# Kernel tuning notes

Hardware: AMD Instinct MI355X
Metric: run time of the kernel (lower is better)

Reference implementation:

```python
import jax, jax.numpy as jnp
import numpy as np

N_LAYERS = 4
H = 16
LOOKBACK = 128  # cross_window
EPS = 1e-6
ROPE_BASE = 10000.0
NEG = jnp.float32(-1e30)


def rmsnorm(x, w):
    return x * jax.lax.rsqrt(jnp.mean(x * x, axis=-1, keepdims=True) + EPS) * w


def rope_cache(L, hd):
    inv = 1.0 / (ROPE_BASE ** (jnp.arange(0, hd, 2, dtype=jnp.float32) / hd))
    t = jnp.arange(L, dtype=jnp.float32)
    f = t[:, None] * inv[None, :]            # [L, hd/2]
    emb = jnp.concatenate([f, f], axis=-1)   # [L, hd]
    return jnp.cos(emb), jnp.sin(emb)


def apply_rope(x, cos, sin):
    # x: [B,H,L,d]; rotate-half convention
    d = x.shape[-1]
    x1, x2 = x[..., : d // 2], x[..., d // 2:]
    rot = jnp.concatenate([-x2, x1], axis=-1)
    return x * cos + rot * sin


def split_heads(x, n_heads):
    B, L, D = x.shape
    return x.reshape(B, L, n_heads, D // n_heads).transpose(0, 2, 1, 3)


def merge_heads(x):
    B, h, L, d = x.shape
    return x.transpose(0, 2, 1, 3).reshape(B, L, h * d)


def sdpa(q, k, v, bias):
    scale = q.shape[-1] ** -0.5
    s = jnp.einsum('bhqd,bhkd->bhqk', q, k) * scale + bias
    p = jax.nn.softmax(s, axis=-1)
    return jnp.einsum('bhqk,bhkd->bhqd', p, v)


def forward(x, memory, seg_ids, Wqkv, bqkv, Wo, bo, Wq_c, Wkv_c, Wo_c, Wg, Wu, Wd, n1, n2, n3, nf):
    B, L, D = x.shape
    S = memory.shape[1]
    hd = D // H
    cos, sin = rope_cache(L, hd)

    # causal additive mask [1,1,L,L]
    i = jnp.arange(L)
    causal_bias = jnp.where(i[None, :] <= i[:, None], 0.0, NEG)[None, None]

    # segment-causal sliding-window cross mask [B,1,L,S]:
    # token t may attend memory j with seg_id[t]-LOOKBACK < j <= seg_id[t]
    j = jnp.arange(S)
    allowed = (j[None, None, :] <= seg_ids[:, :, None]) & (j[None, None, :] > seg_ids[:, :, None] - LOOKBACK)
    cross_bias = jnp.where(allowed, 0.0, NEG)[:, None]  # [B,1,L,S]

    for l in range(N_LAYERS):
        # --- causal self-attn with RoPE ---
        h = rmsnorm(x, n1[l])
        qkv = h @ Wqkv[l].T + bqkv[l]                      # [B,L,3D]
        q, k, v = jnp.split(qkv, 3, axis=-1)
        q = apply_rope(split_heads(q, H), cos, sin)
        k = apply_rope(split_heads(k, H), cos, sin)
        v = split_heads(v, H)
        o = merge_heads(sdpa(q, k, v, causal_bias)) @ Wo[l].T + bo[l]
        x = x + o

        # --- segment-causal sliding-window cross-attn ---
        h2 = rmsnorm(x, n2[l])
        qc = split_heads(h2 @ Wq_c[l].T, H)
        kv = memory @ Wkv_c[l].T                           # [B,S,2D]
        kc, vc = jnp.split(kv, 2, axis=-1)
        kc, vc = split_heads(kc, H), split_heads(vc, H)
        oc = merge_heads(sdpa(qc, kc, vc, cross_bias)) @ Wo_c[l].T
        x = x + oc

        # --- SwiGLU FFN ---
        h3 = rmsnorm(x, n3[l])
        x = x + (jax.nn.silu(h3 @ Wg[l].T) * (h3 @ Wu[l].T)) @ Wd[l].T

    return rmsnorm(x, nf)


def setup_inputs() -> dict:
    key = jax.random.key(0)
    ks = jax.random.split(key, 16)
    B, L, S, D, F = 2, 2048, 256, 1024, 4096
    w = 0.02
    inp = {
        'x': jax.random.normal(ks[0], (B, L, D), jnp.float32),
        'memory': jax.random.normal(ks[1], (B, S, D), jnp.float32),
        'seg_ids': jnp.sort(jax.random.randint(ks[2], (B, L), 0, S), axis=-1),
        'Wqkv': jax.random.normal(ks[3], (N_LAYERS, 3 * D, D), jnp.float32) * w,
        'bqkv': jnp.zeros((N_LAYERS, 3 * D), jnp.float32),
        'Wo': jax.random.normal(ks[4], (N_LAYERS, D, D), jnp.float32) * w,
        'bo': jnp.zeros((N_LAYERS, D), jnp.float32),
        'Wq_c': jax.random.normal(ks[5], (N_LAYERS, D, D), jnp.float32) * w,
        'Wkv_c': jax.random.normal(ks[6], (N_LAYERS, 2 * D, D), jnp.float32) * w,
        'Wo_c': jax.random.normal(ks[7], (N_LAYERS, D, D), jnp.float32) * w,
        'Wg': jax.random.normal(ks[8], (N_LAYERS, F, D), jnp.float32) * w,
        'Wu': jax.random.normal(ks[9], (N_LAYERS, F, D), jnp.float32) * w,
        'Wd': jax.random.normal(ks[10], (N_LAYERS, D, F), jnp.float32) * w,
        'n1': jnp.ones((N_LAYERS, D), jnp.float32),
        'n2': jnp.ones((N_LAYERS, D), jnp.float32),
        'n3': jnp.ones((N_LAYERS, D), jnp.float32),
        'nf': jnp.ones((D,), jnp.float32),
    }
    return inp


def reference(x, memory, seg_ids, Wqkv, bqkv, Wo, bo, Wq_c, Wkv_c, Wo_c, Wg, Wu, Wd, n1, n2, n3, nf):
    return forward(x, memory, seg_ids, Wqkv, bqkv, Wo, bo, Wq_c, Wkv_c, Wo_c, Wg, Wu, Wd, n1, n2, n3, nf)
```

## Files before the change

### kernel.cpp

```cpp
#include <hip/hip_runtime.h>
#include <hip/hip_bf16.h>
#include <math.h>

#define N_LAYERS 4
#define NHEADS 16
#define LOOKBACK 128

typedef unsigned short ushort_t;
typedef __attribute__((ext_vector_type(8))) short short8;
typedef __attribute__((ext_vector_type(4))) float f32x4;

__device__ __forceinline__ ushort_t f2bf(float f) {
    union { float f; unsigned int u; } v; v.f = f;
    unsigned int r = (v.u + 0x7FFFu + ((v.u >> 16) & 1u)) >> 16;
    return (ushort_t)r;
}
__device__ __forceinline__ float bf2f(ushort_t s) {
    union { unsigned int u; float f; } v; v.u = ((unsigned int)s) << 16;
    return v.f;
}

__device__ __forceinline__ float blk_sum(float v, volatile float* red) {
#pragma unroll
    for (int o = 32; o > 0; o >>= 1) v += __shfl_down(v, o, 64);
    if ((threadIdx.x & 63) == 0) red[threadIdx.x >> 6] = v;
    __syncthreads();
    float r = red[0] + red[1] + red[2] + red[3];
    __syncthreads();
    return r;
}

__global__ __launch_bounds__(256) void f2b_k(const float* __restrict__ in,
                                             ushort_t* __restrict__ out, int n4) {
    int i = blockIdx.x * 256 + threadIdx.x;
    if (i >= n4) return;
    float4 v = *(const float4*)(in + (size_t)i * 4);
    ushort_t* o = out + (size_t)i * 4;
    o[0] = f2bf(v.x); o[1] = f2bf(v.y); o[2] = f2bf(v.z); o[3] = f2bf(v.w);
}

__global__ __launch_bounds__(256) void rmsnorm_bf(const float* __restrict__ x,
                                                  const float* __restrict__ w,
                                                  ushort_t* __restrict__ out, int D) {
    __shared__ float red[4];
    size_t row = blockIdx.x;
    const float* xr = x + row * D;
    float ss = 0.f;
    for (int i = threadIdx.x; i < D; i += 256) { float v = xr[i]; ss += v * v; }
    float tot = blk_sum(ss, red);
    float r = rsqrtf(tot / (float)D + 1e-6f);
    ushort_t* o = out + row * D;
    for (int i = threadIdx.x; i < D; i += 256) o[i] = f2bf(xr[i] * r * w[i]);
}

__global__ __launch_bounds__(256) void rmsnorm_k(const float* __restrict__ x,
                                                 const float* __restrict__ w,
                                                 float* __restrict__ out, int D) {
    __shared__ float red[4];
    size_t row = blockIdx.x;
    const float* xr = x + row * D;
    float ss = 0.f;
    for (int i = threadIdx.x; i < D; i += 256) { float v = xr[i]; ss += v * v; }
    float tot = blk_sum(ss, red);
    float r = rsqrtf(tot / (float)D + 1e-6f);
    float* o = out + row * D;
    for (int i = threadIdx.x; i < D; i += 256) o[i] = xr[i] * r * w[i];
}

#define GBM 128
#define GBN 128
#define GBK 32

__global__ __launch_bounds__(256) void gemm_bf16(
    const ushort_t* __restrict__ A, const ushort_t* __restrict__ Bw,
    void* __restrict__ Cout, const float* __restrict__ bias,
    const float* __restrict__ resid, const ushort_t* __restrict__ gate,
    int M, int N, int K, int out_bf16) {
    __shared__ ushort_t As[GBM * GBK];
    __shared__ ushort_t Bs[GBN * GBK];
    int tid = threadIdx.x;
    int wave = tid >> 6, lane = tid & 63;
    int bm = blockIdx.y * GBM, bn = blockIdx.x * GBN;
    int wm = (wave & 1) * 64, wn = (wave >> 1) * 64;
    int r4 = lane >> 2, c4 = lane & 3;
    int r = lane & 15, q = lane >> 4;

    f32x4 acc[4][4];
#pragma unroll
    for (int i = 0; i < 4; ++i)
#pragma unroll
        for (int j = 0; j < 4; ++j) acc[i][j] = (f32x4){0.f, 0.f, 0.f, 0.f};

    int srow = wave * 16 + r4;
    for (int k0 = 0; k0 < K; k0 += GBK) {
        const ushort_t* Ag = A + (size_t)(bm + srow) * K + k0 + c4 * 8;
        const ushort_t* Bg = Bw + (size_t)(bn + srow) * K + k0 + c4 * 8;
        __builtin_amdgcn_global_load_lds(
            (const __attribute__((address_space(1))) void*)Ag,
            (__attribute__((address_space(3))) void*)&As[wave * 16 * GBK],
            16, 0, 0);
        __builtin_amdgcn_global_load_lds(
            (const __attribute__((address_space(1))) void*)(Ag + (size_t)64 * K),
            (__attribute__((address_space(3))) void*)&As[(64 + wave * 16) * GBK],
            16, 0, 0);
        __builtin_amdgcn_global_load_lds(
            (const __attribute__((address_space(1))) void*)Bg,
            (__attribute__((address_space(3))) void*)&Bs[wave * 16 * GBK],
            16, 0, 0);
        __builtin_amdgcn_global_load_lds(
            (const __attribute__((address_space(1))) void*)(Bg + (size_t)64 * K),
            (__attribute__((address_space(3))) void*)&Bs[(64 + wave * 16) * GBK],
            16, 0, 0);
        __syncthreads();
        short8 af[4], bfr[4];
#pragma unroll
        for (int i = 0; i < 4; ++i)
            af[i] = *(const short8*)&As[(wm + 16 * i + r) * GBK + q * 8];
#pragma unroll
        for (int j = 0; j < 4; ++j)
            bfr[j] = *(const short8*)&Bs[(wn + 16 * j + r) * GBK + q * 8];
#pragma unroll
        for (int i = 0; i < 4; ++i)
#pragma unroll
            for (int j = 0; j < 4; ++j)
                acc[i][j] = __builtin_amdgcn_mfma_f32_16x16x32_bf16(
                    af[i], bfr[j], acc[i][j], 0, 0, 0);
        __syncthreads();
    }
#pragma unroll
    for (int i = 0; i < 4; ++i) {
#pragma unroll
        for (int j = 0; j < 4; ++j) {
            size_t n = (size_t)(bn + wn + 16 * j + r);
            float bn_v = bias ? bias[n] : 0.f;
#pragma unroll
            for (int t = 0; t < 4; ++t) {
                size_t m = (size_t)(bm + wm + 16 * i + q * 4 + t);
                size_t idx = m * N + n;
                float x = acc[i][j][t] + bn_v;
                if (gate) { float g = bf2f(gate[idx]); x *= g / (1.0f + __expf(-g)); }
                if (resid) x += resid[idx];
                if (out_bf16) ((ushort_t*)Cout)[idx] = f2bf(x);
                else ((float*)Cout)[idx] = x;
            }
        }
    }
}

__global__ void rope_k(ushort_t* __restrict__ qkv, int L, int total) {
    int idx = blockIdx.x * 256 + threadIdx.x;
    if (idx >= total) return;
    int d = idx & 31;
    int h = (idx >> 5) & 15;
    int bl = idx >> 9;
    int l = bl % L;
    float inv = powf(10000.0f, -(float)d * (1.0f / 32.0f));
    float f = (float)l * inv;
    float s, c;
    sincosf(f, &s, &c);
    ushort_t* base = qkv + (size_t)bl * 3072 + h * 64 + d;
    float x1 = bf2f(base[0]), x2 = bf2f(base[32]);
    base[0]  = f2bf((x1 * c - x2 * s) * 0.125f);
    base[32] = f2bf((x2 * c + x1 * s) * 0.125f);
    ushort_t* kb = base + 1024;
    x1 = bf2f(kb[0]); x2 = bf2f(kb[32]);
    kb[0]  = f2bf(x1 * c - x2 * s);
    kb[32] = f2bf(x2 * c + x1 * s);
}

#define AP 72

__global__ __launch_bounds__(256) void self_attn_flash(
    const ushort_t* __restrict__ qkv, ushort_t* __restrict__ out, int L) {
    int qt = blockIdx.x, h = blockIdx.y, b = blockIdx.z;
    int q0 = qt * 64;
    __shared__ ushort_t Qs[64 * AP];
    __shared__ ushort_t Ks[64 * AP];
    __shared__ ushort_t VT[64 * AP];
    __shared__ ushort_t Ps[64 * AP];
    int tid = threadIdx.x;
    int wave = tid >> 6, lane = tid & 63;
    int g = lane >> 4, r = lane & 15;
    int lr = tid >> 2, lc = tid & 3;

    {
        const ushort_t* src = qkv + ((size_t)b * L + q0 + lr) * 3072 + h * 64 + lc * 16;
        *(short8*)&Qs[lr * AP + lc * 16]     = *(const short8*)(src);
        *(short8*)&Qs[lr * AP + lc * 16 + 8] = *(const short8*)(src + 8);
    }

    float m[4]    = {-1e30f, -1e30f, -1e30f, -1e30f};
    float lsum[4] = {0.f, 0.f, 0.f, 0.f};
    f32x4 acc[4];
#pragma unroll
    for (int j = 0; j < 4; ++j) acc[j] = (f32x4){0.f, 0.f, 0.f, 0.f};

    for (int kt = 0; kt <= qt; ++kt) {
        int k0 = kt * 64;
        __syncthreads();
        {
            const ushort_t* ksrc = qkv + ((size_t)b * L + k0 + lr) * 3072 + 1024 + h * 64 + lc * 16;
            short8 k0v = *(const short8*)(ksrc);
            short8 k1v = *(const short8*)(ksrc + 8);
            *(short8*)&Ks[lr * AP + lc * 16]     = k0v;
            *(short8*)&Ks[lr * AP + lc * 16 + 8] = k1v;
            const ushort_t* vsrc = ksrc + 1024;
            short8 v0v = *(const short8*)(vsrc);
            short8 v1v = *(const short8*)(vsrc + 8);
#pragma unroll
            for (int i = 0; i < 8; ++i) {
                VT[(lc * 16 + i) * AP + lr]     = (ushort_t)v0v[i];
                VT[(lc * 16 + 8 + i) * AP + lr] = (ushort_t)v1v[i];
            }
        }
        __syncthreads();

        f32x4 s[4];
#pragma unroll
        for (int j = 0; j < 4; ++j) s[j] = (f32x4){0.f, 0.f, 0.f, 0.f};
        short8 aq[2];
#pragma unroll
        for (int c = 0; c < 2; ++c)
            aq[c] = *(const short8*)&Qs[(wave * 16 + r) * AP + c * 32 + g * 8];
#pragma unroll
        for (int j = 0; j < 4; ++j)
#pragma unroll
            for (int c = 0; c < 2; ++c) {
                short8 bk = *(const short8*)&Ks[(16 * j + r) * AP + c * 32 + g * 8];
                s[j] = __builtin_amdgcn_mfma_f32_16x16x32_bf16(aq[c], bk, s[j], 0, 0, 0);
            }

        if (kt == qt) {
#pragma unroll
            for (int j = 0; j < 4; ++j)
#pragma unroll
                for (int t = 0; t < 4; ++t)
                    if (16 * j + r > 16 * wave + 4 * g + t) s[j][t] = -1e30f;
        }

        float al[4];
#pragma unroll
        for (int t = 0; t < 4; ++t) {
            float rm = fmaxf(fmaxf(s[0][t], s[1][t]), fmaxf(s[2][t], s[3][t]));
#pragma unroll
            for (int o = 8; o > 0; o >>= 1) rm = fmaxf(rm, __shfl_xor(rm, o, 16));
            float mn = fmaxf(m[t], rm);
            al[t] = __expf(m[t] - mn);
            m[t] = mn;
            float rs = 0.f;
#pragma unroll
            for (int j = 0; j < 4; ++j) {
                float p = __expf(s[j][t] - mn);
                s[j][t] = p;
                rs += p;
            }
#pragma unroll
            for (int o = 8; o > 0; o >>= 1) rs += __shfl_xor(rs, o, 16);
            lsum[t] = lsum[t] * al[t] + rs;
        }

        ushort_t* pw = &Ps[wave * 16 * AP];
#pragma unroll
        for (int j = 0; j < 4; ++j)
#pragma unroll
            for (int t = 0; t < 4; ++t)
                pw[(4 * g + t) * AP + 16 * j + r] = f2bf(s[j][t]);
        short8 ap[2];
#pragma unroll
        for (int c = 0; c < 2; ++c)
            ap[c] = *(const short8*)&pw[r * AP + c * 32 + g * 8];

#pragma unroll
        for (int j = 0; j < 4; ++j) {
#pragma unroll
            for (int t = 0; t < 4; ++t) acc[j][t] *= al[t];
#pragma unroll
            for (int c = 0; c < 2; ++c) {
                short8 bv = *(const short8*)&VT[(16 * j + r) * AP + c * 32 + g * 8];
                acc[j] = __builtin_amdgcn_mfma_f32_16x16x32_bf16(ap[c], bv, acc[j], 0, 0, 0);
            }
        }
    }

#pragma unroll
    for (int t = 0; t < 4; ++t) {
        float invl = 1.0f / lsum[t];
        size_t orow = ((size_t)b * L + q0 + wave * 16 + 4 * g + t) * 1024 + h * 64;
#pragma unroll
        for (int j = 0; j < 4; ++j)
            out[orow + 16 * j + r] = f2bf(acc[j][t] * invl);
    }
}

__global__ __launch_bounds__(256) void cross_attn_mfma(
    const ushort_t* __restrict__ qc, const ushort_t* __restrict__ kvc,
    const int* __restrict__ seg_ids, ushort_t* __restrict__ out, int L, int S) {
    int qt = blockIdx.x, h = blockIdx.y, b = blockIdx.z;
    int q0 = qt * 64;
    __shared__ ushort_t Qs[64 * AP];
    __shared__ ushort_t Ks[64 * AP];
    __shared__ ushort_t VT[64 * AP];
    __shared__ ushort_t Ps[64 * AP];
    __shared__ int segs[64];
    __shared__ int bounds[2];
    int tid = threadIdx.x;
    int wave = tid >> 6, lane = tid & 63;
    int g = lane >> 4, r = lane & 15;
    int lr = tid >> 2, lc = tid & 3;

    {
        const ushort_t* src = qc + ((size_t)b * L + q0 + lr) * 1024 + h * 64 + lc * 16;
        *(short8*)&Qs[lr * AP + lc * 16]     = *(const short8*)(src);
        *(short8*)&Qs[lr * AP + lc * 16 + 8] = *(const short8*)(src + 8);
    }
    if (tid < 64) segs[tid] = seg_ids[(size_t)b * L + q0 + tid];
    __syncthreads();
    if (wave == 0) {
        int v = segs[lane];
        int mn = v, mx = v;
#pragma unroll
        for (int o = 32; o > 0; o >>= 1) {
            mn = min(mn, __shfl_down(mn, o, 64));
            mx = max(mx, __shfl_down(mx, o, 64));
        }
        if (lane == 0) { bounds[0] = mn; bounds[1] = mx; }
    }
    int seg_t[4];
#pragma unroll
    for (int t = 0; t < 4; ++t) seg_t[t] = segs[wave * 16 + 4 * g + t];
    short8 aq[2];
#pragma unroll
    for (int c = 0; c < 2; ++c)
        aq[c] = *(const short8*)&Qs[(wave * 16 + r) * AP + c * 32 + g * 8];
    __syncthreads();
    int lo = bounds[0] - (LOOKBACK - 1); if (lo < 0) lo = 0;
    int t_lo = lo >> 6;
    int t_hi = bounds[1] >> 6;

    float m[4]    = {-1e30f, -1e30f, -1e30f, -1e30f};
    float lsum[4] = {0.f, 0.f, 0.f, 0.f};
    f32x4 acc[4];
#pragma unroll
    for (int j = 0; j < 4; ++j) acc[j] = (f32x4){0.f, 0.f, 0.f, 0.f};

    for (int kt = t_lo; kt <= t_hi; ++kt) {
        int k0 = kt * 64;
        __syncthreads();
        {
            const ushort_t* ksrc = kvc + ((size_t)b * S + k0 + lr) * 2048 + h * 64 + lc * 16;
            short8 k0v = *(const short8*)(ksrc);
            short8 k1v = *(const short8*)(ksrc + 8);
            *(short8*)&Ks[lr * AP + lc * 16]     = k0v;
            *(short8*)&Ks[lr * AP + lc * 16 + 8] = k1v;
            const ushort_t* vsrc = ksrc + 1024;
            short8 v0v = *(const short8*)(vsrc);
            short8 v1v = *(const short8*)(vsrc + 8);
#pragma unroll
            for (int i = 0; i < 8; ++i) {
                VT[(lc * 16 + i) * AP + lr]     = (ushort_t)v0v[i];
                VT[(lc * 16 + 8 + i) * AP + lr] = (ushort_t)v1v[i];
            }
        }
        __syncthreads();

        f32x4 s[4];
#pragma unroll
        for (int j = 0; j < 4; ++j) s[j] = (f32x4){0.f, 0.f, 0.f, 0.f};
#pragma unroll
        for (int j = 0; j < 4; ++j)
#pragma unroll
            for (int c = 0; c < 2; ++c) {
                short8 bk = *(const short8*)&Ks[(16 * j + r) * AP + c * 32 + g * 8];
                s[j] = __builtin_amdgcn_mfma_f32_16x16x32_bf16(aq[c], bk, s[j], 0, 0, 0);
            }

#pragma unroll
        for (int j = 0; j < 4; ++j) {
            int k = k0 + 16 * j + r;
#pragma unroll
            for (int t = 0; t < 4; ++t) {
                float v = s[j][t] * 0.125f;
                if (k > seg_t[t] || k <= seg_t[t] - LOOKBACK) v = -1e30f;
                s[j][t] = v;
            }
        }

        float al[4];
#pragma unroll
        for (int t = 0; t < 4; ++t) {
            float rm = fmaxf(fmaxf(s[0][t], s[1][t]), fmaxf(s[2][t], s[3][t]));
#pragma unroll
            for (int o = 8; o > 0; o >>= 1) rm = fmaxf(rm, __shfl_xor(rm, o, 16));
            float mn = fmaxf(m[t], rm);
            al[t] = __expf(m[t] - mn);
            m[t] = mn;
            float rs = 0.f;
#pragma unroll
            for (int j = 0; j < 4; ++j) {
                float p = __expf(s[j][t] - mn);
                s[j][t] = p;
                rs += p;
            }
#pragma unroll
            for (int o = 8; o > 0; o >>= 1) rs += __shfl_xor(rs, o, 16);
            lsum[t] = lsum[t] * al[t] + rs;
        }

        ushort_t* pw = &Ps[wave * 16 * AP];
#pragma unroll
        for (int j = 0; j < 4; ++j)
#pragma unroll
            for (int t = 0; t < 4; ++t)
                pw[(4 * g + t) * AP + 16 * j + r] = f2bf(s[j][t]);
        short8 ap[2];
#pragma unroll
        for (int c = 0; c < 2; ++c)
            ap[c] = *(const short8*)&pw[r * AP + c * 32 + g * 8];

#pragma unroll
        for (int j = 0; j < 4; ++j) {
#pragma unroll
            for (int t = 0; t < 4; ++t) acc[j][t] *= al[t];
#pragma unroll
            for (int c = 0; c < 2; ++c) {
                short8 bv = *(const short8*)&VT[(16 * j + r) * AP + c * 32 + g * 8];
                acc[j] = __builtin_amdgcn_mfma_f32_16x16x32_bf16(ap[c], bv, acc[j], 0, 0, 0);
            }
        }
    }

#pragma unroll
    for (int t = 0; t < 4; ++t) {
        float invl = 1.0f / lsum[t];
        size_t orow = ((size_t)b * L + q0 + wave * 16 + 4 * g + t) * 1024 + h * 64;
#pragma unroll
        for (int j = 0; j < 4; ++j)
            out[orow + 16 * j + r] = f2bf(acc[j][t] * invl);
    }
}

extern "C" void kernel_launch(void* const* d_in, const int* in_sizes, int n_in,
                              void* d_out, int out_size, void* d_ws, size_t ws_size,
                              hipStream_t stream) {
    const int B = 2, L = 2048, S = 256, D = 1024, F = 4096;
    const int BL = B * L;
    const float* x_in   = (const float*)d_in[0];
    const float* memory = (const float*)d_in[1];
    const int*   seg    = (const int*)d_in[2];
    const float* Wqkv = (const float*)d_in[3];
    const float* bqkv = (const float*)d_in[4];
    const float* Wo   = (const float*)d_in[5];
    const float* bo   = (const float*)d_in[6];
    const float* Wq_c = (const float*)d_in[7];
    const float* Wkv_c= (const float*)d_in[8];
    const float* Wo_c = (const float*)d_in[9];
    const float* Wg   = (const float*)d_in[10];
    const float* Wu   = (const float*)d_in[11];
    const float* Wd   = (const float*)d_in[12];
    const float* n1   = (const float*)d_in[13];
    const float* n2   = (const float*)d_in[14];
    const float* n3   = (const float*)d_in[15];
    const float* nf   = (const float*)d_in[16];

    char* ws = (char*)d_ws;
    size_t off = 0;
    float* X     = (float*)(ws + off); off += (size_t)BL * D * 4;
    float* QKV   = (float*)(ws + off); off += (size_t)BL * 3 * D * 4;
    float* KVC   = (float*)(ws + off); off += (size_t)B * S * 2 * D * 4;
    ushort_t* Hn  = (ushort_t*)(ws + off); off += (size_t)BL * D * 2;
    ushort_t* Abf = (ushort_t*)(ws + off); off += (size_t)BL * D * 2;
    ushort_t* Mb  = (ushort_t*)(ws + off); off += (size_t)B * S * D * 2;
    ushort_t* Wb  = (ushort_t*)(ws + off); off += (size_t)F * D * 2;
    ushort_t* QKVb = (ushort_t*)QKV;
    ushort_t* Qcb  = (ushort_t*)QKV;
    ushort_t* KVCb = (ushort_t*)KVC;
    ushort_t* Gg = (ushort_t*)QKV;

    hipMemcpyAsync(X, x_in, (size_t)BL * D * sizeof(float), hipMemcpyDeviceToDevice, stream);

    dim3 blk(256);
    f2b_k<<<(B * S * D / 4 + 255) / 256, blk, 0, stream>>>(memory, Mb, B * S * D / 4);

    for (int l = 0; l < N_LAYERS; ++l) {
        rmsnorm_bf<<<BL, blk, 0, stream>>>(X, n1 + (size_t)l * D, Hn, D);
        f2b_k<<<(3 * D * D / 4 + 255) / 256, blk, 0, stream>>>(
            Wqkv + (size_t)l * 3 * D * D, Wb, 3 * D * D / 4);
        gemm_bf16<<<dim3(3 * D / GBN, BL / GBM), blk, 0, stream>>>(
            Hn, Wb, QKVb, bqkv + (size_t)l * 3 * D, nullptr, nullptr, BL, 3 * D, D, 1);
        int total = BL * NHEADS * 32;
        rope_k<<<(total + 255) / 256, blk, 0, stream>>>(QKVb, L, total);
        self_attn_flash<<<dim3(L / 64, NHEADS, B), blk, 0, stream>>>(QKVb, Abf, L);
        f2b_k<<<(D * D / 4 + 255) / 256, blk, 0, stream>>>(
            Wo + (size_t)l * D * D, Wb, D * D / 4);
        gemm_bf16<<<dim3(D / GBN, BL / GBM), blk, 0, stream>>>(
            Abf, Wb, X, bo + (size_t)l * D, X, nullptr, BL, D, D, 0);
        rmsnorm_bf<<<BL, blk, 0, stream>>>(X, n2 + (size_t)l * D, Hn, D);
        f2b_k<<<(D * D / 4 + 255) / 256, blk, 0, stream>>>(
            Wq_c + (size_t)l * D * D, Wb, D * D / 4);
        gemm_bf16<<<dim3(D / GBN, BL / GBM), blk, 0, stream>>>(
            Hn, Wb, Qcb, nullptr, nullptr, nullptr, BL, D, D, 1);
        f2b_k<<<(2 * D * D / 4 + 255) / 256, blk, 0, stream>>>(
            Wkv_c + (size_t)l * 2 * D * D, Wb, 2 * D * D / 4);
        gemm_bf16<<<dim3(2 * D / GBN, B * S / GBM), blk, 0, stream>>>(
            Mb, Wb, KVCb, nullptr, nullptr, nullptr, B * S, 2 * D, D, 1);
        cross_attn_mfma<<<dim3(L / 64, NHEADS, B), blk, 0, stream>>>(
            Qcb, KVCb, seg, Abf, L, S);
        f2b_k<<<(D * D / 4 + 255) / 256, blk, 0, stream>>>(
            Wo_c + (size_t)l * D * D, Wb, D * D / 4);
        gemm_bf16<<<dim3(D / GBN, BL / GBM), blk, 0, stream>>>(
            Abf, Wb, X, nullptr, X, nullptr, BL, D, D, 0);
        rmsnorm_bf<<<BL, blk, 0, stream>>>(X, n3 + (size_t)l * D, Hn, D);
        f2b_k<<<(F * D / 4 + 255) / 256, blk, 0, stream>>>(
            Wg + (size_t)l * F * D, Wb, F * D / 4);
        gemm_bf16<<<dim3(F / GBN, BL / GBM), blk, 0, stream>>>(
            Hn, Wb, Gg, nullptr, nullptr, nullptr, BL, F, D, 1);
        f2b_k<<<(F * D / 4 + 255) / 256, blk, 0, stream>>>(
            Wu + (size_t)l * F * D, Wb, F * D / 4);
        gemm_bf16<<<dim3(F / GBN, BL / GBM), blk, 0, stream>>>(
            Hn, Wb, Gg, nullptr, nullptr, Gg, BL, F, D, 1);
        f2b_k<<<(D * F / 4 + 255) / 256, blk, 0, stream>>>(
            Wd + (size_t)l * D * F, Wb, D * F / 4);
        gemm_bf16<<<dim3(D / GBN, BL / GBM), blk, 0, stream>>>(
            Gg, Wb, X, nullptr, X, nullptr, BL, D, F, 0);
    }
    rmsnorm_k<<<BL, blk, 0, stream>>>(X, nf, (float*)d_out, D);
}
```

Measured before the change: 3.021 ms.

## Enlarge self-attention query tile, prefetch KV, swizzle LDS, and remap blocks to XCDs

The self-attention kernel now processes 128 query rows per block, with each wave owning 32 rows, so every K/V tile loaded into LDS is reused twice as much. The next K/V tile is prefetched into registers while the current one is consumed, and the V-transpose and P buffers use XOR-swizzled layouts instead of padding to reduce LDS bank conflicts. Block indices in both the GEMM and the attention kernel are remapped so that neighbouring tiles land on the same XCD for L2 locality. RoPE's powf is replaced with exp2f. The attention remap hardcodes 16 query tiles and 16 heads, which ties it to L=2048, and the larger tile halves the number of attention blocks while raising register pressure.

```diff
diff --git a/kernel.cpp b/kernel.cpp
--- a/kernel.cpp
+++ b/kernel.cpp
@@ -80,7 +80,12 @@
     __shared__ ushort_t Bs[GBN * GBK];
     int tid = threadIdx.x;
     int wave = tid >> 6, lane = tid & 63;
-    int bm = blockIdx.y * GBM, bn = blockIdx.x * GBN;
+    int nwg = gridDim.x * gridDim.y;
+    int wg  = blockIdx.y * gridDim.x + blockIdx.x;
+    int qq = nwg >> 3, rr = nwg & 7;
+    int xcd = wg & 7, loc = wg >> 3;
+    int swz = (xcd < rr ? xcd * (qq + 1) : rr * (qq + 1) + (xcd - rr) * qq) + loc;
+    int bm = (swz / gridDim.x) * GBM, bn = (swz % gridDim.x) * GBN;
     int wm = (wave & 1) * 64, wn = (wave >> 1) * 64;
     int r4 = lane >> 2, c4 = lane & 3;
     int r = lane & 15, q = lane >> 4;
@@ -154,7 +159,7 @@
     int h = (idx >> 5) & 15;
     int bl = idx >> 9;
     int l = bl % L;
-    float inv = powf(10000.0f, -(float)d * (1.0f / 32.0f));
+    float inv = exp2f(-(float)d * (13.2877123795f / 32.0f));
     float f = (float)l * inv;
     float s, c;
     sincosf(f, &s, &c);
@@ -168,129 +173,185 @@
     kb[32] = f2bf(x2 * c + x1 * s);
 }
 
-#define AP 72
+#define QB 128
 
 __global__ __launch_bounds__(256) void self_attn_flash(
     const ushort_t* __restrict__ qkv, ushort_t* __restrict__ out, int L) {
-    int qt = blockIdx.x, h = blockIdx.y, b = blockIdx.z;
-    int q0 = qt * 64;
-    __shared__ ushort_t Qs[64 * AP];
-    __shared__ ushort_t Ks[64 * AP];
-    __shared__ ushort_t VT[64 * AP];
-    __shared__ ushort_t Ps[64 * AP];
+    int lin = blockIdx.x + gridDim.x * (blockIdx.y + gridDim.y * blockIdx.z);
+    int xcd = lin & 7, slot = lin >> 3;
+    int qt = slot & 15;
+    int grp = xcd + 8 * (slot >> 4);
+    int h = grp & 15, b = grp >> 4;
+    int q0 = qt * QB;
+
+    __shared__ ushort_t Qs[QB * 72];
+    __shared__ ushort_t Ks[64 * 72];
+    __shared__ ushort_t VT[64 * 64];
+    __shared__ ushort_t Ps[QB * 64];
+
     int tid = threadIdx.x;
     int wave = tid >> 6, lane = tid & 63;
     int g = lane >> 4, r = lane & 15;
+    int lr2 = tid >> 1, lc2 = tid & 1;
     int lr = tid >> 2, lc = tid & 3;
 
     {
-        const ushort_t* src = qkv + ((size_t)b * L + q0 + lr) * 3072 + h * 64 + lc * 16;
-        *(short8*)&Qs[lr * AP + lc * 16]     = *(const short8*)(src);
-        *(short8*)&Qs[lr * AP + lc * 16 + 8] = *(const short8*)(src + 8);
-    }
-
-    float m[4]    = {-1e30f, -1e30f, -1e30f, -1e30f};
-    float lsum[4] = {0.f, 0.f, 0.f, 0.f};
-    f32x4 acc[4];
-#pragma unroll
-    for (int j = 0; j < 4; ++j) acc[j] = (f32x4){0.f, 0.f, 0.f, 0.f};
-
-    for (int kt = 0; kt <= qt; ++kt) {
+        const ushort_t* src = qkv + ((size_t)b * L + q0 + lr2) * 3072 + h * 64 + lc2 * 32;
+        ushort_t* dst = &Qs[lr2 * 72 + lc2 * 32];
+        *(short8*)(dst)      = *(const short8*)(src);
+        *(short8*)(dst + 8)  = *(const short8*)(src + 8);
+        *(short8*)(dst + 16) = *(const short8*)(src + 16);
+        *(short8*)(dst + 24) = *(const short8*)(src + 24);
+    }
+    __syncthreads();
+    short8 aq[2][2];
+#pragma unroll
+    for (int s = 0; s < 2; ++s)
+#pragma unroll
+        for (int c = 0; c < 2; ++c)
+            aq[s][c] = *(const short8*)&Qs[(wave * 32 + s * 16 + r) * 72 + c * 32 + g * 8];
+
+    const ushort_t* kvbase = qkv + ((size_t)b * L + lr) * 3072 + 1024 + h * 64 + lc * 16;
+    short8 kreg0 = *(const short8*)(kvbase);
+    short8 kreg1 = *(const short8*)(kvbase + 8);
+    short8 vreg0 = *(const short8*)(kvbase + 1024);
+    short8 vreg1 = *(const short8*)(kvbase + 1032);
+
+    float m[2][4], lsum[2][4];
+    f32x4 acc[2][4];
+#pragma unroll
+    for (int s = 0; s < 2; ++s)
+#pragma unroll
+        for (int t = 0; t < 4; ++t) { m[s][t] = -1e30f; lsum[s][t] = 0.f; }
+#pragma unroll
+    for (int s = 0; s < 2; ++s)
+#pragma unroll
+        for (int j = 0; j < 4; ++j) acc[s][j] = (f32x4){0.f, 0.f, 0.f, 0.f};
+
+    int ktmax = 2 * qt + 1;
+    for (int kt = 0; kt <= ktmax; ++kt) {
+        __syncthreads();
+        *(short8*)&Ks[lr * 72 + lc * 16]     = kreg0;
+        *(short8*)&Ks[lr * 72 + lc * 16 + 8] = kreg1;
+#pragma unroll
+        for (int i = 0; i < 8; ++i) {
+            int row0 = lc * 16 + i;
+            int f0 = (row0 & 7) ^ ((row0 >> 4) & 3);
+            VT[row0 * 64 + (((lr >> 3) ^ f0) << 3) + (lr & 7)] = (ushort_t)vreg0[i];
+            int row1 = row0 + 8;
+            int f1 = (row1 & 7) ^ ((row1 >> 4) & 3);
+            VT[row1 * 64 + (((lr >> 3) ^ f1) << 3) + (lr & 7)] = (ushort_t)vreg1[i];
+        }
+        if (kt < ktmax) {
+            const ushort_t* p = kvbase + (size_t)(kt + 1) * 64 * 3072;
+            kreg0 = *(const short8*)(p);
+            kreg1 = *(const short8*)(p + 8);
+            vreg0 = *(const short8*)(p + 1024);
+            vreg1 = *(const short8*)(p + 1032);
+        }
+        __syncthreads();
+
         int k0 = kt * 64;
-        __syncthreads();
-        {
-            const ushort_t* ksrc = qkv + ((size_t)b * L + k0 + lr) * 3072 + 1024 + h * 64 + lc * 16;
-            short8 k0v = *(const short8*)(ksrc);
-            short8 k1v = *(const short8*)(ksrc + 8);
-            *(short8*)&Ks[lr * AP + lc * 16]     = k0v;
-            *(short8*)&Ks[lr * AP + lc * 16 + 8] = k1v;
-            const ushort_t* vsrc = ksrc + 1024;
-            short8 v0v = *(const short8*)(vsrc);
-            short8 v1v = *(const short8*)(vsrc + 8);
-#pragma unroll
-            for (int i = 0; i < 8; ++i) {
-                VT[(lc * 16 + i) * AP + lr]     = (ushort_t)v0v[i];
-                VT[(lc * 16 + 8 + i) * AP + lr] = (ushort_t)v1v[i];
-            }
-        }
-        __syncthreads();
-
-        f32x4 s[4];
-#pragma unroll
-        for (int j = 0; j < 4; ++j) s[j] = (f32x4){0.f, 0.f, 0.f, 0.f};
-        short8 aq[2];
-#pragma unroll
-        for (int c = 0; c < 2; ++c)
-            aq[c] = *(const short8*)&Qs[(wave * 16 + r) * AP + c * 32 + g * 8];
+        f32x4 s2[2][4];
+#pragma unroll
+        for (int s = 0; s < 2; ++s)
+#pragma unroll
+            for (int j = 0; j < 4; ++j) s2[s][j] = (f32x4){0.f, 0.f, 0.f, 0.f};
 #pragma unroll
         for (int j = 0; j < 4; ++j)
 #pragma unroll
             for (int c = 0; c < 2; ++c) {
-                short8 bk = *(const short8*)&Ks[(16 * j + r) * AP + c * 32 + g * 8];
-                s[j] = __builtin_amdgcn_mfma_f32_16x16x32_bf16(aq[c], bk, s[j], 0, 0, 0);
-            }
-
-        if (kt == qt) {
+                short8 bk = *(const short8*)&Ks[(16 * j + r) * 72 + c * 32 + g * 8];
+                s2[0][j] = __builtin_amdgcn_mfma_f32_16x16x32_bf16(aq[0][c], bk, s2[0][j], 0, 0, 0);
+                s2[1][j] = __builtin_amdgcn_mfma_f32_16x16x32_bf16(aq[1][c], bk, s2[1][j], 0, 0, 0);
+            }
+
+        if (kt >= ktmax - 1) {
+#pragma unroll
+            for (int s = 0; s < 2; ++s)
+#pragma unroll
+                for (int j = 0; j < 4; ++j) {
+                    int k = k0 + 16 * j + r;
+#pragma unroll
+                    for (int t = 0; t < 4; ++t)
+                        if (k > q0 + wave * 32 + s * 16 + 4 * g + t) s2[s][j][t] = -1e30f;
+                }
+        }
+
+        float al[2][4];
+#pragma unroll
+        for (int s = 0; s < 2; ++s)
+#pragma unroll
+            for (int t = 0; t < 4; ++t) {
+                float rm = fmaxf(fmaxf(s2[s][0][t], s2[s][1][t]), fmaxf(s2[s][2][t], s2[s][3][t]));
+#pragma unroll
+                for (int o = 8; o > 0; o >>= 1) rm = fmaxf(rm, __shfl_xor(rm, o, 16));
+                float mn = fmaxf(m[s][t], rm);
+                al[s][t] = __expf(m[s][t] - mn);
+                m[s][t] = mn;
+                float rs = 0.f;
+#pragma unroll
+                for (int j = 0; j < 4; ++j) {
+                    float p = __expf(s2[s][j][t] - mn);
+                    s2[s][j][t] = p;
+                    rs += p;
+                }
+#pragma unroll
+                for (int o = 8; o > 0; o >>= 1) rs += __shfl_xor(rs, o, 16);
+                lsum[s][t] = lsum[s][t] * al[s][t] + rs;
+            }
+
+#pragma unroll
+        for (int s = 0; s < 2; ++s)
 #pragma unroll
             for (int j = 0; j < 4; ++j)
 #pragma unroll
-                for (int t = 0; t < 4; ++t)
-                    if (16 * j + r > 16 * wave + 4 * g + t) s[j][t] = -1e30f;
-        }
-
-        float al[4];
+                for (int t = 0; t < 4; ++t) {
+                    int row = wave * 32 + s * 16 + 4 * g + t;
+                    int f = (row >> 1) & 7;
+                    Ps[row * 64 + (((2 * j + (r >> 3)) ^ f) << 3) + (r & 7)] = f2bf(s2[s][j][t]);
+                }
+        short8 ap[2][2];
+#pragma unroll
+        for (int s = 0; s < 2; ++s) {
+            int row = wave * 32 + s * 16 + r;
+            int f = (row >> 1) & 7;
+#pragma unroll
+            for (int c = 0; c < 2; ++c)
+                ap[s][c] = *(const short8*)&Ps[row * 64 + (((4 * c + g) ^ f) << 3)];
+        }
+
+#pragma unroll
+        for (int s = 0; s < 2; ++s)
+#pragma unroll
+            for (int j = 0; j < 4; ++j)
+#pragma unroll
+                for (int t = 0; t < 4; ++t) acc[s][j][t] *= al[s][t];
+#pragma unroll
+        for (int j = 0; j < 4; ++j)
+#pragma unroll
+            for (int c = 0; c < 2; ++c) {
+                int row = 16 * j + r;
+                int ch = (4 * c + g) ^ (r & 7) ^ j;
+                short8 bv = *(const short8*)&VT[row * 64 + (ch << 3)];
+                acc[0][j] = __builtin_amdgcn_mfma_f32_16x16x32_bf16(ap[0][c], bv, acc[0][j], 0, 0, 0);
+                acc[1][j] = __builtin_amdgcn_mfma_f32_16x16x32_bf16(ap[1][c], bv, acc[1][j], 0, 0, 0);
+            }
+    }
+
+#pragma unroll
+    for (int s = 0; s < 2; ++s)
 #pragma unroll
         for (int t = 0; t < 4; ++t) {
-            float rm = fmaxf(fmaxf(s[0][t], s[1][t]), fmaxf(s[2][t], s[3][t]));
-#pragma unroll
-            for (int o = 8; o > 0; o >>= 1) rm = fmaxf(rm, __shfl_xor(rm, o, 16));
-            float mn = fmaxf(m[t], rm);
-            al[t] = __expf(m[t] - mn);
-            m[t] = mn;
-            float rs = 0.f;
-#pragma unroll
-            for (int j = 0; j < 4; ++j) {
-                float p = __expf(s[j][t] - mn);
-                s[j][t] = p;
-                rs += p;
-            }
-#pragma unroll
-            for (int o = 8; o > 0; o >>= 1) rs += __shfl_xor(rs, o, 16);
-            lsum[t] = lsum[t] * al[t] + rs;
-        }
-
-        ushort_t* pw = &Ps[wave * 16 * AP];
-#pragma unroll
-        for (int j = 0; j < 4; ++j)
-#pragma unroll
-            for (int t = 0; t < 4; ++t)
-                pw[(4 * g + t) * AP + 16 * j + r] = f2bf(s[j][t]);
-        short8 ap[2];
-#pragma unroll
-        for (int c = 0; c < 2; ++c)
-            ap[c] = *(const short8*)&pw[r * AP + c * 32 + g * 8];
-
-#pragma unroll
-        for (int j = 0; j < 4; ++j) {
-#pragma unroll
-            for (int t = 0; t < 4; ++t) acc[j][t] *= al[t];
-#pragma unroll
-            for (int c = 0; c < 2; ++c) {
-                short8 bv = *(const short8*)&VT[(16 * j + r) * AP + c * 32 + g * 8];
-                acc[j] = __builtin_amdgcn_mfma_f32_16x16x32_bf16(ap[c], bv, acc[j], 0, 0, 0);
-            }
-        }
-    }
-
-#pragma unroll
-    for (int t = 0; t < 4; ++t) {
-        float invl = 1.0f / lsum[t];
-        size_t orow = ((size_t)b * L + q0 + wave * 16 + 4 * g + t) * 1024 + h * 64;
-#pragma unroll
-        for (int j = 0; j < 4; ++j)
-            out[orow + 16 * j + r] = f2bf(acc[j][t] * invl);
-    }
-}
+            float invl = 1.0f / lsum[s][t];
+            size_t orow = ((size_t)b * L + q0 + wave * 32 + s * 16 + 4 * g + t) * 1024 + h * 64;
+#pragma unroll
+            for (int j = 0; j < 4; ++j)
+                out[orow + 16 * j + r] = f2bf(acc[s][j][t] * invl);
+        }
+}
+
+#define AP 72
 
 __global__ __launch_bounds__(256) void cross_attn_mfma(
     const ushort_t* __restrict__ qc, const ushort_t* __restrict__ kvc,
@@ -489,7 +550,7 @@
             Hn, Wb, QKVb, bqkv + (size_t)l * 3 * D, nullptr, nullptr, BL, 3 * D, D, 1);
         int total = BL * NHEADS * 32;
         rope_k<<<(total + 255) / 256, blk, 0, stream>>>(QKVb, L, total);
-        self_attn_flash<<<dim3(L / 64, NHEADS, B), blk, 0, stream>>>(QKVb, Abf, L);
+        self_attn_flash<<<dim3(L / QB, NHEADS, B), blk, 0, stream>>>(QKVb, Abf, L);
         f2b_k<<<(D * D / 4 + 255) / 256, blk, 0, stream>>>(
             Wo + (size_t)l * D * D, Wb, D * D / 4);
         gemm_bf16<<<dim3(D / GBN, BL / GBM), blk, 0, stream>>>(
```

After: 2.864 ms. 1.05x faster.
